# Kernel optimization log

Measured on AMD Instinct MI355X. Metric: run time of the kernel, lower is better.

The kernel has to match this reference:

```python
import jax, jax.numpy as jnp
import numpy as np

B, N, D = 8, 2048, 768
LN_EPS = 1e-5


def setup_inputs() -> dict:
    key = jax.random.key(0)
    ks = jax.random.split(key, 5)
    scale = 1.0 / np.sqrt(D)
    features = jax.random.normal(ks[0], (B, N, D), dtype=jnp.float32)
    mask = jax.random.randint(ks[1], (B, N), 0, 2) == 1  # True = masked (padding)
    Wq = jax.random.normal(ks[2], (D, D), dtype=jnp.float32) * scale
    Wk = jax.random.normal(ks[3], (D, D), dtype=jnp.float32) * scale
    Wv = jax.random.normal(ks[4], (D, D), dtype=jnp.float32) * scale
    ln_gamma = jnp.ones((D,), dtype=jnp.float32)
    ln_beta = jnp.zeros((D,), dtype=jnp.float32)
    return {"features": features, "mask": mask, "Wq": Wq, "Wk": Wk, "Wv": Wv,
            "ln_gamma": ln_gamma, "ln_beta": ln_beta}


def reference(features, mask, Wq, Wk, Wv, ln_gamma, ln_beta):
    # LayerNorm over last dim
    mu = jnp.mean(features, axis=-1, keepdims=True)
    var = jnp.mean(jnp.square(features - mu), axis=-1, keepdims=True)
    x = (features - mu) * jax.lax.rsqrt(var + LN_EPS) * ln_gamma + ln_beta
    # torch Linear: y = x @ W.T
    Q = jnp.einsum('bnd,ed->bne', x, Wq)
    K = jnp.einsum('bnd,ed->bne', x, Wk)
    V = jnp.einsum('bnd,ed->bne', x, Wv)
    scale = x.shape[-1] ** -0.5
    scores = jnp.einsum('bnd,bmd->bnm', Q, K) * scale  # [B,N,N]
    scores = jnp.where(mask[:, None, :], -jnp.inf, scores)
    probs = jax.nn.softmax(scores, axis=-1)
    ctx = jnp.einsum('bnm,bmd->bnd', probs, V)
    return ctx
```

## Files before the change

kernel.cpp:

```cpp
#include <hip/hip_runtime.h>
#include <hip/hip_bf16.h>
#include <cstdint>

typedef __attribute__((ext_vector_type(8))) __bf16 bf16v8;
typedef __attribute__((ext_vector_type(4))) float f32x4;
typedef __attribute__((ext_vector_type(4))) unsigned short ushort4v;
typedef __attribute__((ext_vector_type(8))) unsigned short ushort8v;

#define BB 8
#define NN 2048
#define DD 768

__device__ __forceinline__ float b2f(unsigned short u) {
  union { unsigned int i; float f; } c; c.i = ((unsigned int)u) << 16; return c.f;
}
__device__ __forceinline__ unsigned short f2b(float f) {
  union { float f; unsigned int i; } c; c.f = f;
  unsigned int u = c.i;
  return (unsigned short)((u + 0x7fffu + ((u >> 16) & 1u)) >> 16);
}

__global__ __launch_bounds__(256) void ln_kernel(const float* __restrict__ x,
                                                 const float* __restrict__ gamma,
                                                 const float* __restrict__ beta,
                                                 unsigned short* __restrict__ xb) {
  int row = blockIdx.x;
  const float* xr = x + (size_t)row * DD;
  int t = threadIdx.x;
  float a0 = xr[t], a1 = xr[t + 256], a2 = xr[t + 512];
  float s = a0 + a1 + a2;
  float q = a0 * a0 + a1 * a1 + a2 * a2;
  for (int o = 32; o > 0; o >>= 1) { s += __shfl_xor(s, o); q += __shfl_xor(q, o); }
  __shared__ float red[2][4];
  int w = t >> 6, lane = t & 63;
  if (lane == 0) { red[0][w] = s; red[1][w] = q; }
  __syncthreads();
  s = red[0][0] + red[0][1] + red[0][2] + red[0][3];
  q = red[1][0] + red[1][1] + red[1][2] + red[1][3];
  float mean = s * (1.0f / DD);
  float var = q * (1.0f / DD) - mean * mean;
  float inv = rsqrtf(var + 1e-5f);
  unsigned short* o0 = xb + (size_t)row * DD;
  o0[t]       = f2b((a0 - mean) * inv * gamma[t]       + beta[t]);
  o0[t + 256] = f2b((a1 - mean) * inv * gamma[t + 256] + beta[t + 256]);
  o0[t + 512] = f2b((a2 - mean) * inv * gamma[t + 512] + beta[t + 512]);
}

__global__ __launch_bounds__(256) void wconvert(const float* __restrict__ Wq,
                                                const float* __restrict__ Wk,
                                                const float* __restrict__ Wv,
                                                unsigned short* __restrict__ Wcat) {
  int i = blockIdx.x * 256 + threadIdx.x;
  const int dd = DD * DD;
  if (i >= 3 * dd) return;
  float v;
  if (i < dd)           v = Wq[i] * 0.03608439182435161f;
  else if (i < 2 * dd)  v = Wk[i - dd];
  else                  v = Wv[i - 2 * dd];
  Wcat[i] = f2b(v);
}

__global__ __launch_bounds__(256) void mask_scan(const int* __restrict__ mask,
                                                 int* __restrict__ kidx,
                                                 int* __restrict__ ncnt) {
  int b = blockIdx.x;
  const int* mr = mask + b * NN;
  int t = threadIdx.x;
#pragma unroll
  for (int j = 0; j < 8; ++j) kidx[b * NN + t * 8 + j] = 0;
  int v[8]; int s = 0;
#pragma unroll
  for (int j = 0; j < 8; ++j) { v[j] = (mr[t * 8 + j] == 0) ? 1 : 0; s += v[j]; }
  int lane = t & 63, w = t >> 6;
  int x = s;
  for (int o = 1; o < 64; o <<= 1) { int y = __shfl_up(x, o); if (lane >= o) x += y; }
  __shared__ int wsum[4];
  if (lane == 63) wsum[w] = x;
  __syncthreads();
  int base = 0;
#pragma unroll
  for (int i = 0; i < 4; ++i) if (i < w) base += wsum[i];
  int run = base + x - s;
#pragma unroll
  for (int j = 0; j < 8; ++j) { if (v[j]) kidx[b * NN + run] = t * 8 + j; run += v[j]; }
  if (t == 255) ncnt[b] = base + x;
}

__global__ __launch_bounds__(256) void xc_gather(const unsigned short* __restrict__ Xb,
                                                 const int* __restrict__ kidx,
                                                 const int* __restrict__ ncnt,
                                                 unsigned short* __restrict__ Xc) {
  const int b = blockIdx.y;
  const int nc = ncnt[b];
  const int r256 = (nc + 255) & ~255;
  const int row0 = blockIdx.x * 16;
  if (row0 >= r256) return;
  int off = 0;
#pragma unroll
  for (int i = 0; i < 8; ++i) if (i < b) off += (ncnt[i] + 255) & ~255;
  for (int u = threadIdx.x; u < 16 * 96; u += 256) {
    const int r = row0 + u / 96;
    const int ch = (u % 96) * 8;
    if (r >= r256) continue;
    ushort8v val = {0, 0, 0, 0, 0, 0, 0, 0};
    if (r < nc)
      val = *(const ushort8v*)&Xb[((size_t)b * NN + kidx[b * NN + r]) * DD + ch];
    *(ushort8v*)&Xc[(size_t)(off + r) * DD + ch] = val;
  }
}

__device__ __forceinline__ void gload_lds16(const void* g, void* l) {
  __builtin_amdgcn_global_load_lds(
      (const __attribute__((address_space(1))) void*)g,
      (__attribute__((address_space(3))) void*)(unsigned)(uintptr_t)l,
      16, 0, 0);
}

#define RDA(i0, ks, B)                                                                   \
  _Pragma("unroll")                                                                      \
  for (int i_ = 0; i_ < 4; ++i_)                                                         \
    aq[i_] = *(const bf16v8*)&smem[(B) + (ks) * 8192 + arow0 + ((i0) + i_) * 512 + kg8];
#define RDB(ks, B)                                                                       \
  _Pragma("unroll")                                                                      \
  for (int j_ = 0; j_ < NJ; ++j_)                                                        \
    bq[j_] = *(const bf16v8*)&smem[(B) + 16384 + (ks) * 8192 + brow0 + j_ * 512 + kg8];
#define MFQ(i0)                                                                          \
  _Pragma("unroll")                                                                      \
  for (int i_ = 0; i_ < 4; ++i_) {                                                       \
    _Pragma("unroll")                                                                    \
    for (int j_ = 0; j_ < NJ; ++j_)                                                      \
      acc[(i0) + i_][j_] = __builtin_amdgcn_mfma_f32_16x16x32_bf16(                      \
          aq[i_], bq[j_], acc[(i0) + i_][j_], 0, 0, 0);                                  \
  }
#define BARF asm volatile("s_barrier" ::: "memory")
#define VMC6 asm volatile("s_waitcnt vmcnt(6)" ::: "memory")
#define VMC3 asm volatile("s_waitcnt vmcnt(3)" ::: "memory")
#define VMC0 asm volatile("s_waitcnt vmcnt(0)" ::: "memory")
#define P1   __builtin_amdgcn_s_setprio(1)
#define P0   __builtin_amdgcn_s_setprio(0)

#define TILEK(KT, CURB, NXTB)                                                            \
  do {                                                                                   \
    RDA(0, 0, CURB); RDB(0, CURB);                                                       \
    if ((KT) + 1 < NT) stgA((KT) + 1, 1, (NXTB));                                        \
    BARF; P1; MFQ(0); P0; BARF;                                                          \
    RDA(4, 0, CURB);                                                                     \
    if ((KT) + 1 < NT) stgB((KT) + 1, 1, (NXTB));                                        \
    BARF; P1; MFQ(4); P0;                                                                \
    VMC6; BARF;                                                                          \
    RDA(0, 1, CURB); RDB(1, CURB);                                                       \
    if ((KT) + 2 < NT) stgA((KT) + 2, 0, (CURB));                                        \
    BARF; P1; MFQ(0); P0; BARF;                                                          \
    RDA(4, 1, CURB);                                                                     \
    if ((KT) + 2 < NT) stgB((KT) + 2, 0, (CURB));                                        \
    BARF; P1; MFQ(4); P0;                                                                \
    if ((KT) < NT - 2) { VMC6; } else { VMC0; }                                          \
    BARF;                                                                                \
  } while (0)

template <int MODE, int NJ>
__global__ __launch_bounds__(512, 2) void gemm256(
    const unsigned short* __restrict__ A, const unsigned short* __restrict__ Bm,
    unsigned short* __restrict__ Cq, float* __restrict__ Cf,
    int K, int lda, int ldb,
    long aStride, long bStride, long cStride,
    const int* __restrict__ ncnt) {
  extern __shared__ unsigned short smem[];
  const int BN = NJ * 64;

  const int t = threadIdx.x;
  int bx = blockIdx.x, by = blockIdx.y, bz = blockIdx.z;
  {
    const int gx = gridDim.x, gy = gridDim.y;
    const int nwg = gx * gy * (int)gridDim.z;
    int id = bx + gx * (by + gy * bz);
    int sw = (id & 7) * (nwg >> 3) + (id >> 3);
    bx = sw % gx; int r2 = sw / gx;
    by = r2 % gy; bz = r2 / gy;
  }
  const int n0 = bx * BN, m0 = by * 256;
  const int NT = (MODE == 2) ? (((ncnt[bz] + 127) >> 7) << 1) : (K >> 6);

  const unsigned short* Ab = A + (size_t)bz * aStride;
  const unsigned short* Bb = Bm + (size_t)bz * bStride;

  const int lane = t & 63;
  const int w = t >> 6;
  const int wm = w >> 2, wn = w & 3;
  const int frow = lane & 15;
  const int kg8 = (lane >> 4) * 8;
  const int arow0 = (wm * 128 + frow) * 32;
  const int brow0 = (wn * (NJ * 16) + frow) * 32;

  const int srow = t >> 2;
  const int scol8 = (t & 3) * 8;
  const unsigned short* Asrc = Ab + (size_t)(m0 + srow) * lda + scol8;
  const unsigned short* Bsrc = Bb + (size_t)(n0 + srow) * ldb + scol8;
  const int sdst = w * 512;

  auto stgA = [&](int kt, int ks, int bufb) {
    const unsigned short* s = Asrc + kt * 64 + ks * 32;
    gload_lds16(s, &smem[bufb + ks * 8192 + sdst]);
    gload_lds16(s + (size_t)128 * lda, &smem[bufb + ks * 8192 + 4096 + sdst]);
  };
  auto stgB = [&](int kt, int ks, int bufb) {
    const unsigned short* s = Bsrc + kt * 64 + ks * 32;
    gload_lds16(s, &smem[bufb + 16384 + ks * 8192 + sdst]);
    gload_lds16(s + (size_t)128 * ldb, &smem[bufb + 16384 + ks * 8192 + 4096 + sdst]);
  };

  f32x4 acc[8][NJ] = {};
  bf16v8 aq[4], bq[NJ];

  stgA(0, 0, 0);     stgB(0, 0, 0);
  stgA(0, 1, 0);     stgB(0, 1, 0);
  stgA(1, 0, 32768); stgB(1, 0, 32768);
  asm volatile("s_waitcnt vmcnt(8)" ::: "memory");
  BARF;

  for (int ktp = 0; ktp < NT; ktp += 2) {
    TILEK(ktp, 0, 32768);
    TILEK(ktp + 1, 32768, 0);
  }

  const int r0 = (lane >> 4) * 4;
  const int c0 = lane & 15;
  const int mrowB = m0 + wm * 128 + r0;
  const int ncolB = n0 + wn * (NJ * 16) + c0;

  if (MODE == 3) {
#pragma unroll
    for (int i = 0; i < 8; ++i)
#pragma unroll
      for (int j = 0; j < NJ; ++j)
#pragma unroll
        for (int r = 0; r < 4; ++r)
          Cq[(size_t)(mrowB + i * 16 + r) * DD + (ncolB + j * 16)] = f2b(acc[i][j][r]);
  } else {
    float* dst = Cf + (size_t)bz * cStride;
#pragma unroll
    for (int i = 0; i < 8; ++i)
#pragma unroll
      for (int j = 0; j < NJ; ++j)
#pragma unroll
        for (int r = 0; r < 4; ++r)
          dst[(size_t)(mrowB + i * 16 + r) * DD + (ncolB + j * 16)] = acc[i][j][r];
  }
}

template <int NJ, int NTT>
__global__ __launch_bounds__(512, 2) void gemmKV(
    const unsigned short* __restrict__ Xc, const unsigned short* __restrict__ Wcat,
    unsigned short* __restrict__ Kc, unsigned short* __restrict__ Vtc,
    const int* __restrict__ ncnt) {
  extern __shared__ unsigned short smem[];
  constexpr int NT = NTT;

  int offv[9]; offv[0] = 0;
#pragma unroll
  for (int i = 0; i < 8; ++i) offv[i + 1] = offv[i] + ((ncnt[i] + 255) & ~255);
  const int GT = offv[8] >> 8;
  const int id = (int)blockIdx.x;
  if (id >= GT * 8) return;
  const int gt = id >> 3, ni = id & 7;
  int b = 0;
#pragma unroll
  for (int i = 1; i < 8; ++i) if (offv[i] <= gt * 256) b = i;
  const int off_b = offv[b];

  const int t = threadIdx.x;
  const int lane = t & 63;
  const int w = t >> 6;
  const int wm = w >> 2, wn = w & 3;
  const int frow = lane & 15;
  const int kg8 = (lane >> 4) * 8;
  const int arow0 = (wm * 128 + frow) * 32;
  const int brow0 = (wn * (NJ * 16) + frow) * 32;
  const int srow = t >> 2;
  const int scol8 = (t & 3) * 8;
  const int sdst = w * 512;

  const unsigned short* Asrc = Xc + (size_t)(gt * 256 + srow) * DD + scol8;
  const unsigned short* Bsrc = Wcat + (size_t)(768 + ni * (NJ * 64) + srow) * DD + scol8;

  auto stgA = [&](int kt, int ks, int bufb) {
    const unsigned short* s = Asrc + kt * 64 + ks * 32;
    gload_lds16(s, &smem[bufb + ks * 8192 + sdst]);
    gload_lds16(s + (size_t)128 * DD, &smem[bufb + ks * 8192 + 4096 + sdst]);
  };
  auto stgB = [&](int kt, int ks, int bufb) {
    const unsigned short* s = Bsrc + kt * 64 + ks * 32;
    gload_lds16(s, &smem[bufb + 16384 + ks * 8192 + sdst]);
    gload_lds16(s + (size_t)128 * DD, &smem[bufb + 16384 + ks * 8192 + 4096 + sdst]);
  };

  f32x4 acc[8][NJ] = {};
  bf16v8 aq[4], bq[NJ];

  stgA(0, 0, 0);     stgB(0, 0, 0);
  stgA(0, 1, 0);     stgB(0, 1, 0);
  stgA(1, 0, 32768); stgB(1, 0, 32768);
  asm volatile("s_waitcnt vmcnt(8)" ::: "memory");
  BARF;

  for (int ktp = 0; ktp < NT; ktp += 2) {
    TILEK(ktp, 0, 32768);
    TILEK(ktp + 1, 32768, 0);
  }

  const int r0 = (lane >> 4) * 4;
  const int c0 = lane & 15;
  const int rowL = wm * 128 + r0;
  const int ncolL = ni * (NJ * 64) + wn * (NJ * 16) + c0;
  const int cbase = gt * 256 - off_b + rowL;

  if (ni < 4) {
    unsigned short* dst = Kc + (size_t)b * NN * DD;
#pragma unroll
    for (int i = 0; i < 8; ++i)
#pragma unroll
      for (int j = 0; j < NJ; ++j)
#pragma unroll
        for (int r = 0; r < 4; ++r)
          dst[(size_t)(cbase + i * 16 + r) * DD + (ncolL + j * 16)] = f2b(acc[i][j][r]);
  } else {
#pragma unroll
    for (int i = 0; i < 8; ++i) {
#pragma unroll
      for (int j = 0; j < NJ; ++j) {
        const int e = ncolL + j * 16 - 768;
        ushort4v pk;
#pragma unroll
        for (int r = 0; r < 4; ++r) pk[r] = f2b(acc[i][j][r]);
        *(ushort4v*)&Vtc[((size_t)b * DD + e) * NN + cbase + i * 16] = pk;
      }
    }
  }
}

__global__ __launch_bounds__(512, 2) void gemm1P(
    const unsigned short* __restrict__ Qa, const unsigned short* __restrict__ Kn,
    unsigned short* __restrict__ So, const int* __restrict__ ncnt) {
  extern __shared__ unsigned short smem[];
  constexpr int NT = 12;

  const int t = threadIdx.x;
  const int lane = t & 63;
  const int w = t >> 6;
  const int wm = w >> 2, wn = w & 3;
  const int frow = lane & 15;
  const int kg8 = (lane >> 4) * 8;
  const int arow0 = (wm * 64 + frow) * 32;
  const int brow0 = (wn * 64 + frow) * 32;
  const int srow = t >> 2;
  const int scol8 = (t & 3) * 8;
  const int sdst = w * 512;
  const int r0 = (lane >> 4) * 4;
  const int c0 = lane & 15;

  int nbv[8];
#pragma unroll
  for (int b_ = 0; b_ < 8; ++b_) nbv[b_] = (ncnt[b_] + 255) >> 8;

  f32x4 acc[4][4];
  bf16v8 aq[4], bq[4];

#pragma unroll 1
  for (int it = 0; it < 4; ++it) {
    int rem = (int)blockIdx.x + it * 256;
    int b = 0;
#pragma unroll 1
    for (; b < 8; ++b) { int c = nbv[b] * 16; if (rem < c) break; rem -= c; }
    if (b >= 8) break;
    const int ni = rem >> 4, mi = rem & 15;
    const int m0 = mi * 128, n0 = ni * 256;

    const unsigned short* Asrc = Qa + ((size_t)b * NN + m0 + srow) * DD + scol8;
    const unsigned short* Bsrc = Kn + ((size_t)b * NN + n0 + srow) * DD + scol8;

    auto stgA = [&](int kt, int ks, int bufb) {
      gload_lds16(Asrc + kt * 64 + ks * 32, &smem[bufb + ks * 4096 + sdst]);
    };
    auto stgB = [&](int kt, int ks, int bufb) {
      const unsigned short* s = Bsrc + kt * 64 + ks * 32;
      gload_lds16(s, &smem[bufb + 8192 + ks * 8192 + sdst]);
      gload_lds16(s + (size_t)128 * DD, &smem[bufb + 8192 + ks * 8192 + 4096 + sdst]);
    };

#pragma unroll
    for (int i = 0; i < 4; ++i)
#pragma unroll
      for (int j = 0; j < 4; ++j) acc[i][j] = f32x4{0.f, 0.f, 0.f, 0.f};

    stgA(0, 0, 0);     stgB(0, 0, 0);
    stgA(0, 1, 0);     stgB(0, 1, 0);
    stgA(1, 0, 24576); stgB(1, 0, 24576);
    VMC3;
    BARF;

#pragma unroll 1
    for (int kt = 0; kt < NT; ++kt) {
      const int cur = (kt & 1) ? 24576 : 0;
      const int nxt = cur ^ 24576;
#pragma unroll
      for (int i_ = 0; i_ < 4; ++i_)
        aq[i_] = *(const bf16v8*)&smem[cur + arow0 + i_ * 512 + kg8];
#pragma unroll
      for (int j_ = 0; j_ < 4; ++j_)
        bq[j_] = *(const bf16v8*)&smem[cur + 8192 + brow0 + j_ * 512 + kg8];
      if (kt + 1 < NT) { stgA(kt + 1, 1, nxt); stgB(kt + 1, 1, nxt); }
      BARF; P1;
#pragma unroll
      for (int i_ = 0; i_ < 4; ++i_)
#pragma unroll
        for (int j_ = 0; j_ < 4; ++j_)
          acc[i_][j_] = __builtin_amdgcn_mfma_f32_16x16x32_bf16(aq[i_], bq[j_], acc[i_][j_], 0, 0, 0);
      P0; BARF;
#pragma unroll
      for (int i_ = 0; i_ < 4; ++i_)
        aq[i_] = *(const bf16v8*)&smem[cur + 4096 + arow0 + i_ * 512 + kg8];
#pragma unroll
      for (int j_ = 0; j_ < 4; ++j_)
        bq[j_] = *(const bf16v8*)&smem[cur + 16384 + brow0 + j_ * 512 + kg8];
      if (kt + 2 < NT) { stgA(kt + 2, 0, cur); stgB(kt + 2, 0, cur); }
      BARF; P1;
#pragma unroll
      for (int i_ = 0; i_ < 4; ++i_)
#pragma unroll
        for (int j_ = 0; j_ < 4; ++j_)
          acc[i_][j_] = __builtin_amdgcn_mfma_f32_16x16x32_bf16(aq[i_], bq[j_], acc[i_][j_], 0, 0, 0);
      P0;
      if (kt < NT - 2) { VMC3; } else { VMC0; }
      BARF;
    }

    unsigned short* dst = So + (size_t)b * NN * NN;
    const int mrowB = m0 + wm * 64 + r0;
    const int ncolB = n0 + wn * 64 + c0;
#pragma unroll
    for (int i = 0; i < 4; ++i)
#pragma unroll
      for (int j = 0; j < 4; ++j)
#pragma unroll
        for (int r = 0; r < 4; ++r)
          dst[(size_t)(mrowB + i * 16 + r) * NN + (ncolB + j * 16)] = f2b(acc[i][j][r]);
  }
}

__global__ __launch_bounds__(256) void softmax_c(unsigned short* __restrict__ S,
                                                 const int* __restrict__ ncnt) {
  int row = blockIdx.x;
  int bb = row >> 11;
  const int nc = ncnt[bb];
  const int p128 = (nc + 127) & ~127;
  unsigned short* sr = S + (size_t)row * NN;
  int t = threadIdx.x;
  const int cbase = t * 8;

  float v[8];
  const bool anyload = cbase < nc;
  ushort8v pk;
  if (anyload) pk = *(const ushort8v*)&sr[cbase];
  float mx = -1e30f;
#pragma unroll
  for (int j = 0; j < 8; ++j) {
    v[j] = anyload ? b2f(pk[j]) : 0.f;
    if (cbase + j < nc) mx = fmaxf(mx, v[j]);
  }
  for (int o = 32; o > 0; o >>= 1) mx = fmaxf(mx, __shfl_xor(mx, o));
  __shared__ float redm[4], reds[4];
  int w = t >> 6, lane = t & 63;
  if (lane == 0) redm[w] = mx;
  __syncthreads();
  mx = fmaxf(fmaxf(redm[0], redm[1]), fmaxf(redm[2], redm[3]));

  float e[8];
  float sum = 0.f;
#pragma unroll
  for (int j = 0; j < 8; ++j) {
    e[j] = (cbase + j < nc) ? __expf(v[j] - mx) : 0.f;
    sum += e[j];
  }
  for (int o = 32; o > 0; o >>= 1) sum += __shfl_xor(sum, o);
  if (lane == 0) reds[w] = sum;
  __syncthreads();
  sum = reds[0] + reds[1] + reds[2] + reds[3];
  float inv = 1.0f / sum;

  if (cbase < p128) {
    ushort8v op;
#pragma unroll
    for (int j = 0; j < 8; ++j) op[j] = f2b(e[j] * inv);
    *(ushort8v*)&sr[cbase] = op;
  }
}

extern "C" void kernel_launch(void* const* d_in, const int* in_sizes, int n_in,
                              void* d_out, int out_size, void* d_ws, size_t ws_size,
                              hipStream_t stream) {
  const float* features = (const float*)d_in[0];
  const int* mask       = (const int*)d_in[1];
  const float* Wq       = (const float*)d_in[2];
  const float* Wk       = (const float*)d_in[3];
  const float* Wv       = (const float*)d_in[4];
  const float* gamma    = (const float*)d_in[5];
  const float* beta     = (const float*)d_in[6];
  float* out = (float*)d_out;

  char* ws = (char*)d_ws;
  size_t off = 0;
  auto alloc = [&](size_t bytes) {
    char* p = ws + off;
    off += (bytes + 255) & ~(size_t)255;
    return p;
  };
  unsigned short* Wcat = (unsigned short*)alloc((size_t)(2304 + 64) * DD * 2);
  unsigned short* Qb   = (unsigned short*)alloc((size_t)BB * NN * DD * 2);
  unsigned short* Kc   = (unsigned short*)alloc((size_t)BB * NN * DD * 2);
  unsigned short* Vtc  = (unsigned short*)alloc(((size_t)BB * DD + 64) * NN * 2);
  int* kidx = (int*)alloc((size_t)BB * NN * 4);
  int* ncnt = (int*)alloc(64 * 4);
  char* last = alloc((size_t)BB * NN * NN * 2);
  unsigned short* Sb = (unsigned short*)last;
  unsigned short* Xb = (unsigned short*)last;
  unsigned short* Xc = (unsigned short*)(last + (size_t)34 * 1024 * 1024);

  (void)hipFuncSetAttribute(reinterpret_cast<const void*>(&gemm256<3, 3>),
                            hipFuncAttributeMaxDynamicSharedMemorySize, 131072);
  (void)hipFuncSetAttribute(reinterpret_cast<const void*>(&gemmKV<3, 12>),
                            hipFuncAttributeMaxDynamicSharedMemorySize, 131072);
  (void)hipFuncSetAttribute(reinterpret_cast<const void*>(&gemm1P),
                            hipFuncAttributeMaxDynamicSharedMemorySize, 98304);
  (void)hipFuncSetAttribute(reinterpret_cast<const void*>(&gemm256<2, 3>),
                            hipFuncAttributeMaxDynamicSharedMemorySize, 131072);

  ln_kernel<<<BB * NN, 256, 0, stream>>>(features, gamma, beta, Xb);
  wconvert<<<(3 * DD * DD + 255) / 256, 256, 0, stream>>>(Wq, Wk, Wv, Wcat);
  mask_scan<<<BB, 256, 0, stream>>>(mask, kidx, ncnt);
  xc_gather<<<dim3(128, BB), 256, 0, stream>>>(Xb, kidx, ncnt, Xc);

  gemm256<3, 3><<<dim3(4, 64, 1), 512, 131072, stream>>>(
      Xb, Wcat, Qb, nullptr, DD, DD, DD, 0, 0, 0, ncnt);

  gemmKV<3, 12><<<512, 512, 131072, stream>>>(Xc, Wcat, Kc, Vtc, ncnt);

  gemm1P<<<256, 512, 98304, stream>>>(Qb, Kc, Sb, ncnt);

  softmax_c<<<BB * NN, 256, 0, stream>>>(Sb, ncnt);

  gemm256<2, 3><<<dim3(DD / 192, NN / 256, BB), 512, 131072, stream>>>(
      Sb, Vtc, nullptr, out, NN, NN, NN,
      (long)NN * NN, (long)DD * NN, (long)NN * DD, ncnt);
}
```

Baseline: 217.4 us.

## Fuse prep kernels into one launch and merge Q and KV projections

Combines layernorm, weight conversion and mask scan into a single block-indexed prep kernel. It also merges the separate Q projection GEMM and the compacted K/V projection GEMM into one launch with 768 blocks, where the first 256 compute Q and the rest compute K/V. This removes launch gaps and tail idle time between small kernels and lets Q and KV work share the GPU concurrently. The cost is more divergent code paths inside one kernel, and the prep kernel's single shared-memory footprint applies to every branch.

```diff
diff --git a/kernel.cpp b/kernel.cpp
--- a/kernel.cpp
+++ b/kernel.cpp
@@ -20,70 +20,67 @@
   return (unsigned short)((u + 0x7fffu + ((u >> 16) & 1u)) >> 16);
 }
 
-__global__ __launch_bounds__(256) void ln_kernel(const float* __restrict__ x,
-                                                 const float* __restrict__ gamma,
-                                                 const float* __restrict__ beta,
-                                                 unsigned short* __restrict__ xb) {
-  int row = blockIdx.x;
-  const float* xr = x + (size_t)row * DD;
-  int t = threadIdx.x;
-  float a0 = xr[t], a1 = xr[t + 256], a2 = xr[t + 512];
-  float s = a0 + a1 + a2;
-  float q = a0 * a0 + a1 * a1 + a2 * a2;
-  for (int o = 32; o > 0; o >>= 1) { s += __shfl_xor(s, o); q += __shfl_xor(q, o); }
+__global__ __launch_bounds__(256) void prep(
+    const float* __restrict__ x, const float* __restrict__ gamma, const float* __restrict__ beta,
+    unsigned short* __restrict__ xb,
+    const float* __restrict__ Wq, const float* __restrict__ Wk, const float* __restrict__ Wv,
+    unsigned short* __restrict__ Wcat,
+    const int* __restrict__ mask, int* __restrict__ kidx, int* __restrict__ ncnt) {
   __shared__ float red[2][4];
-  int w = t >> 6, lane = t & 63;
-  if (lane == 0) { red[0][w] = s; red[1][w] = q; }
-  __syncthreads();
-  s = red[0][0] + red[0][1] + red[0][2] + red[0][3];
-  q = red[1][0] + red[1][1] + red[1][2] + red[1][3];
-  float mean = s * (1.0f / DD);
-  float var = q * (1.0f / DD) - mean * mean;
-  float inv = rsqrtf(var + 1e-5f);
-  unsigned short* o0 = xb + (size_t)row * DD;
-  o0[t]       = f2b((a0 - mean) * inv * gamma[t]       + beta[t]);
-  o0[t + 256] = f2b((a1 - mean) * inv * gamma[t + 256] + beta[t + 256]);
-  o0[t + 512] = f2b((a2 - mean) * inv * gamma[t + 512] + beta[t + 512]);
-}
-
-__global__ __launch_bounds__(256) void wconvert(const float* __restrict__ Wq,
-                                                const float* __restrict__ Wk,
-                                                const float* __restrict__ Wv,
-                                                unsigned short* __restrict__ Wcat) {
-  int i = blockIdx.x * 256 + threadIdx.x;
-  const int dd = DD * DD;
-  if (i >= 3 * dd) return;
-  float v;
-  if (i < dd)           v = Wq[i] * 0.03608439182435161f;
-  else if (i < 2 * dd)  v = Wk[i - dd];
-  else                  v = Wv[i - 2 * dd];
-  Wcat[i] = f2b(v);
-}
-
-__global__ __launch_bounds__(256) void mask_scan(const int* __restrict__ mask,
-                                                 int* __restrict__ kidx,
-                                                 int* __restrict__ ncnt) {
-  int b = blockIdx.x;
-  const int* mr = mask + b * NN;
-  int t = threadIdx.x;
-#pragma unroll
-  for (int j = 0; j < 8; ++j) kidx[b * NN + t * 8 + j] = 0;
-  int v[8]; int s = 0;
-#pragma unroll
-  for (int j = 0; j < 8; ++j) { v[j] = (mr[t * 8 + j] == 0) ? 1 : 0; s += v[j]; }
-  int lane = t & 63, w = t >> 6;
-  int x = s;
-  for (int o = 1; o < 64; o <<= 1) { int y = __shfl_up(x, o); if (lane >= o) x += y; }
   __shared__ int wsum[4];
-  if (lane == 63) wsum[w] = x;
-  __syncthreads();
-  int base = 0;
-#pragma unroll
-  for (int i = 0; i < 4; ++i) if (i < w) base += wsum[i];
-  int run = base + x - s;
-#pragma unroll
-  for (int j = 0; j < 8; ++j) { if (v[j]) kidx[b * NN + run] = t * 8 + j; run += v[j]; }
-  if (t == 255) ncnt[b] = base + x;
+  const int bid = blockIdx.x;
+  const int t = threadIdx.x;
+
+  if (bid < BB * NN) {
+    const int row = bid;
+    const float* xr = x + (size_t)row * DD;
+    float a0 = xr[t], a1 = xr[t + 256], a2 = xr[t + 512];
+    float s = a0 + a1 + a2;
+    float q = a0 * a0 + a1 * a1 + a2 * a2;
+    for (int o = 32; o > 0; o >>= 1) { s += __shfl_xor(s, o); q += __shfl_xor(q, o); }
+    int w = t >> 6, lane = t & 63;
+    if (lane == 0) { red[0][w] = s; red[1][w] = q; }
+    __syncthreads();
+    s = red[0][0] + red[0][1] + red[0][2] + red[0][3];
+    q = red[1][0] + red[1][1] + red[1][2] + red[1][3];
+    float mean = s * (1.0f / DD);
+    float var = q * (1.0f / DD) - mean * mean;
+    float inv = rsqrtf(var + 1e-5f);
+    unsigned short* o0 = xb + (size_t)row * DD;
+    o0[t]       = f2b((a0 - mean) * inv * gamma[t]       + beta[t]);
+    o0[t + 256] = f2b((a1 - mean) * inv * gamma[t + 256] + beta[t + 256]);
+    o0[t + 512] = f2b((a2 - mean) * inv * gamma[t + 512] + beta[t + 512]);
+  } else if (bid < BB * NN + 6912) {
+    const int i = (bid - BB * NN) * 256 + t;
+    const int dd = DD * DD;
+    if (i < 3 * dd) {
+      float v;
+      if (i < dd)           v = Wq[i] * 0.03608439182435161f;
+      else if (i < 2 * dd)  v = Wk[i - dd];
+      else                  v = Wv[i - 2 * dd];
+      Wcat[i] = f2b(v);
+    }
+  } else {
+    const int b = bid - (BB * NN + 6912);
+    const int* mr = mask + b * NN;
+#pragma unroll
+    for (int j = 0; j < 8; ++j) kidx[b * NN + t * 8 + j] = 0;
+    int v[8]; int s = 0;
+#pragma unroll
+    for (int j = 0; j < 8; ++j) { v[j] = (mr[t * 8 + j] == 0) ? 1 : 0; s += v[j]; }
+    int lane = t & 63, w = t >> 6;
+    int xp = s;
+    for (int o = 1; o < 64; o <<= 1) { int y = __shfl_up(xp, o); if (lane >= o) xp += y; }
+    if (lane == 63) wsum[w] = xp;
+    __syncthreads();
+    int base = 0;
+#pragma unroll
+    for (int i = 0; i < 4; ++i) if (i < w) base += wsum[i];
+    int run = base + xp - s;
+#pragma unroll
+    for (int j = 0; j < 8; ++j) { if (v[j]) kidx[b * NN + run] = t * 8 + j; run += v[j]; }
+    if (t == 255) ncnt[b] = base + xp;
+  }
 }
 
 __global__ __launch_bounds__(256) void xc_gather(const unsigned short* __restrict__ Xb,
@@ -158,11 +155,10 @@
     BARF;                                                                                \
   } while (0)
 
-template <int MODE, int NJ>
-__global__ __launch_bounds__(512, 2) void gemm256(
+template <int NJ>
+__global__ __launch_bounds__(512, 2) void gemmCtx(
     const unsigned short* __restrict__ A, const unsigned short* __restrict__ Bm,
-    unsigned short* __restrict__ Cq, float* __restrict__ Cf,
-    int K, int lda, int ldb,
+    float* __restrict__ Cf, int lda, int ldb,
     long aStride, long bStride, long cStride,
     const int* __restrict__ ncnt) {
   extern __shared__ unsigned short smem[];
@@ -179,7 +175,7 @@
     by = r2 % gy; bz = r2 / gy;
   }
   const int n0 = bx * BN, m0 = by * 256;
-  const int NT = (MODE == 2) ? (((ncnt[bz] + 127) >> 7) << 1) : (K >> 6);
+  const int NT = ((ncnt[bz] + 127) >> 7) << 1;
 
   const unsigned short* Ab = A + (size_t)bz * aStride;
   const unsigned short* Bb = Bm + (size_t)bz * bStride;
@@ -227,48 +223,28 @@
   const int c0 = lane & 15;
   const int mrowB = m0 + wm * 128 + r0;
   const int ncolB = n0 + wn * (NJ * 16) + c0;
-
-  if (MODE == 3) {
-#pragma unroll
-    for (int i = 0; i < 8; ++i)
-#pragma unroll
-      for (int j = 0; j < NJ; ++j)
-#pragma unroll
-        for (int r = 0; r < 4; ++r)
-          Cq[(size_t)(mrowB + i * 16 + r) * DD + (ncolB + j * 16)] = f2b(acc[i][j][r]);
-  } else {
-    float* dst = Cf + (size_t)bz * cStride;
-#pragma unroll
-    for (int i = 0; i < 8; ++i)
-#pragma unroll
-      for (int j = 0; j < NJ; ++j)
-#pragma unroll
-        for (int r = 0; r < 4; ++r)
-          dst[(size_t)(mrowB + i * 16 + r) * DD + (ncolB + j * 16)] = acc[i][j][r];
-  }
-}
-
-template <int NJ, int NTT>
-__global__ __launch_bounds__(512, 2) void gemmKV(
-    const unsigned short* __restrict__ Xc, const unsigned short* __restrict__ Wcat,
-    unsigned short* __restrict__ Kc, unsigned short* __restrict__ Vtc,
-    const int* __restrict__ ncnt) {
+  float* dst = Cf + (size_t)bz * cStride;
+#pragma unroll
+  for (int i = 0; i < 8; ++i)
+#pragma unroll
+    for (int j = 0; j < NJ; ++j)
+#pragma unroll
+      for (int r = 0; r < 4; ++r)
+        dst[(size_t)(mrowB + i * 16 + r) * DD + (ncolB + j * 16)] = acc[i][j][r];
+}
+
+template <int NJ>
+__global__ __launch_bounds__(512, 2) void gemmQKV(
+    const unsigned short* __restrict__ Xb, const unsigned short* __restrict__ Xc,
+    const unsigned short* __restrict__ Wcat,
+    unsigned short* __restrict__ Qb, unsigned short* __restrict__ Kc,
+    unsigned short* __restrict__ Vtc, const int* __restrict__ ncnt) {
   extern __shared__ unsigned short smem[];
-  constexpr int NT = NTT;
-
-  int offv[9]; offv[0] = 0;
-#pragma unroll
-  for (int i = 0; i < 8; ++i) offv[i + 1] = offv[i] + ((ncnt[i] + 255) & ~255);
-  const int GT = offv[8] >> 8;
+  constexpr int NT = 12;
+
+  const int t = threadIdx.x;
   const int id = (int)blockIdx.x;
-  if (id >= GT * 8) return;
-  const int gt = id >> 3, ni = id & 7;
-  int b = 0;
-#pragma unroll
-  for (int i = 1; i < 8; ++i) if (offv[i] <= gt * 256) b = i;
-  const int off_b = offv[b];
-
-  const int t = threadIdx.x;
+
   const int lane = t & 63;
   const int w = t >> 6;
   const int wm = w >> 2, wn = w & 3;
@@ -280,8 +256,29 @@
   const int scol8 = (t & 3) * 8;
   const int sdst = w * 512;
 
-  const unsigned short* Asrc = Xc + (size_t)(gt * 256 + srow) * DD + scol8;
-  const unsigned short* Bsrc = Wcat + (size_t)(768 + ni * (NJ * 64) + srow) * DD + scol8;
+  const bool isQ = id < 256;
+  const unsigned short* Asrc;
+  const unsigned short* Bsrc;
+  int m0 = 0, ncolQ = 0, b = 0, cbase0 = 0, ni = 0;
+  if (isQ) {
+    m0 = (id >> 2) * 256;
+    ncolQ = (id & 3) * 192;
+    Asrc = Xb + (size_t)(m0 + srow) * DD + scol8;
+    Bsrc = Wcat + (size_t)(ncolQ + srow) * DD + scol8;
+  } else {
+    int offv[9]; offv[0] = 0;
+#pragma unroll
+    for (int i = 0; i < 8; ++i) offv[i + 1] = offv[i] + ((ncnt[i] + 255) & ~255);
+    const int GT = offv[8] >> 8;
+    const int kid = id - 256;
+    if (kid >= GT * 8) return;
+    const int gt = kid >> 3; ni = kid & 7;
+#pragma unroll
+    for (int i = 1; i < 8; ++i) if (offv[i] <= gt * 256) b = i;
+    cbase0 = gt * 256 - offv[b];
+    Asrc = Xc + (size_t)(gt * 256 + srow) * DD + scol8;
+    Bsrc = Wcat + (size_t)(768 + ni * (NJ * 64) + srow) * DD + scol8;
+  }
 
   auto stgA = [&](int kt, int ks, int bufb) {
     const unsigned short* s = Asrc + kt * 64 + ks * 32;
@@ -310,29 +307,40 @@
 
   const int r0 = (lane >> 4) * 4;
   const int c0 = lane & 15;
-  const int rowL = wm * 128 + r0;
-  const int ncolL = ni * (NJ * 64) + wn * (NJ * 16) + c0;
-  const int cbase = gt * 256 - off_b + rowL;
-
-  if (ni < 4) {
-    unsigned short* dst = Kc + (size_t)b * NN * DD;
+  if (isQ) {
+    const int mrowB = m0 + wm * 128 + r0;
+    const int ncolB = ncolQ + wn * (NJ * 16) + c0;
 #pragma unroll
     for (int i = 0; i < 8; ++i)
 #pragma unroll
       for (int j = 0; j < NJ; ++j)
 #pragma unroll
         for (int r = 0; r < 4; ++r)
-          dst[(size_t)(cbase + i * 16 + r) * DD + (ncolL + j * 16)] = f2b(acc[i][j][r]);
+          Qb[(size_t)(mrowB + i * 16 + r) * DD + (ncolB + j * 16)] = f2b(acc[i][j][r]);
   } else {
-#pragma unroll
-    for (int i = 0; i < 8; ++i) {
-#pragma unroll
-      for (int j = 0; j < NJ; ++j) {
-        const int e = ncolL + j * 16 - 768;
-        ushort4v pk;
-#pragma unroll
-        for (int r = 0; r < 4; ++r) pk[r] = f2b(acc[i][j][r]);
-        *(ushort4v*)&Vtc[((size_t)b * DD + e) * NN + cbase + i * 16] = pk;
+    const int rowL = wm * 128 + r0;
+    const int ncolL = ni * (NJ * 64) + wn * (NJ * 16) + c0;
+    const int cbase = cbase0 + rowL;
+    if (ni < 4) {
+      unsigned short* dst = Kc + (size_t)b * NN * DD;
+#pragma unroll
+      for (int i = 0; i < 8; ++i)
+#pragma unroll
+        for (int j = 0; j < NJ; ++j)
+#pragma unroll
+          for (int r = 0; r < 4; ++r)
+            dst[(size_t)(cbase + i * 16 + r) * DD + (ncolL + j * 16)] = f2b(acc[i][j][r]);
+    } else {
+#pragma unroll
+      for (int i = 0; i < 8; ++i) {
+#pragma unroll
+        for (int j = 0; j < NJ; ++j) {
+          const int e = ncolL + j * 16 - 768;
+          ushort4v pk;
+#pragma unroll
+          for (int r = 0; r < 4; ++r) pk[r] = f2b(acc[i][j][r]);
+          *(ushort4v*)&Vtc[((size_t)b * DD + e) * NN + cbase + i * 16] = pk;
+        }
       }
     }
   }
@@ -525,30 +533,25 @@
   unsigned short* Xb = (unsigned short*)last;
   unsigned short* Xc = (unsigned short*)(last + (size_t)34 * 1024 * 1024);
 
-  (void)hipFuncSetAttribute(reinterpret_cast<const void*>(&gemm256<3, 3>),
-                            hipFuncAttributeMaxDynamicSharedMemorySize, 131072);
-  (void)hipFuncSetAttribute(reinterpret_cast<const void*>(&gemmKV<3, 12>),
+  (void)hipFuncSetAttribute(reinterpret_cast<const void*>(&gemmQKV<3>),
                             hipFuncAttributeMaxDynamicSharedMemorySize, 131072);
   (void)hipFuncSetAttribute(reinterpret_cast<const void*>(&gemm1P),
                             hipFuncAttributeMaxDynamicSharedMemorySize, 98304);
-  (void)hipFuncSetAttribute(reinterpret_cast<const void*>(&gemm256<2, 3>),
+  (void)hipFuncSetAttribute(reinterpret_cast<const void*>(&gemmCtx<3>),
                             hipFuncAttributeMaxDynamicSharedMemorySize, 131072);
 
-  ln_kernel<<<BB * NN, 256, 0, stream>>>(features, gamma, beta, Xb);
-  wconvert<<<(3 * DD * DD + 255) / 256, 256, 0, stream>>>(Wq, Wk, Wv, Wcat);
-  mask_scan<<<BB, 256, 0, stream>>>(mask, kidx, ncnt);
+  prep<<<BB * NN + 6912 + BB, 256, 0, stream>>>(
+      features, gamma, beta, Xb, Wq, Wk, Wv, Wcat, mask, kidx, ncnt);
+
   xc_gather<<<dim3(128, BB), 256, 0, stream>>>(Xb, kidx, ncnt, Xc);
 
-  gemm256<3, 3><<<dim3(4, 64, 1), 512, 131072, stream>>>(
-      Xb, Wcat, Qb, nullptr, DD, DD, DD, 0, 0, 0, ncnt);
-
-  gemmKV<3, 12><<<512, 512, 131072, stream>>>(Xc, Wcat, Kc, Vtc, ncnt);
+  gemmQKV<3><<<768, 512, 131072, stream>>>(Xb, Xc, Wcat, Qb, Kc, Vtc, ncnt);
 
   gemm1P<<<256, 512, 98304, stream>>>(Qb, Kc, Sb, ncnt);
 
   softmax_c<<<BB * NN, 256, 0, stream>>>(Sb, ncnt);
 
-  gemm256<2, 3><<<dim3(DD / 192, NN / 256, BB), 512, 131072, stream>>>(
-      Sb, Vtc, nullptr, out, NN, NN, NN,
+  gemmCtx<3><<<dim3(DD / 192, NN / 256, BB), 512, 131072, stream>>>(
+      Sb, Vtc, out, NN, NN,
       (long)NN * NN, (long)DD * NN, (long)NN * DD, ncnt);
 }
```

Result: no change. 213.8 us (-1.7%).
